# Performance work log

Measured on AMD Instinct MI355X. Metric: run time of the kernel, lower is better.

Reference implementation:

```python
import jax, jax.numpy as jnp
import numpy as np

H = 1024  # hidden_size
IN = 1    # input_size
OUT = 1   # out_size


def _lstm_cell(x, h, c, W_ih, W_hh, b_ih, b_hh):
    # PyTorch LSTMCell: gates ordered (i, f, g, o)
    gates = x @ W_ih.T + h @ W_hh.T + (b_ih + b_hh)
    i, f, g, o = jnp.split(gates, 4, axis=-1)
    c_new = jax.nn.sigmoid(f) * c + jax.nn.sigmoid(i) * jnp.tanh(g)
    h_new = jax.nn.sigmoid(o) * jnp.tanh(c_new)
    return h_new, c_new


def setup_inputs() -> dict:
    key = jax.random.key(0)
    ks = jax.random.split(key, 12)
    B, T = 128, 256
    s1 = 1.0 / np.sqrt(H)
    u = lambda k, shp: jax.random.uniform(k, shp, jnp.float32, -s1, s1)
    return {
        "x": jax.random.normal(ks[0], (B, T), jnp.float32),
        "W_ih1": u(ks[1], (4 * H, IN)),
        "W_hh1": u(ks[2], (4 * H, H)),
        "b_ih1": u(ks[3], (4 * H,)),
        "b_hh1": u(ks[4], (4 * H,)),
        "W_ih2": u(ks[5], (4 * H, H)),
        "W_hh2": u(ks[6], (4 * H, H)),
        "b_ih2": u(ks[7], (4 * H,)),
        "b_hh2": u(ks[8], (4 * H,)),
        "W_lin": u(ks[9], (OUT, H)),
        "b_lin": u(ks[10], (OUT,)),
        "future": 64,
    }


def reference(x, W_ih1, W_hh1, b_ih1, b_hh1, W_ih2, W_hh2, b_ih2, b_hh2,
              W_lin, b_lin, future):
    B = x.shape[0]
    z = jnp.zeros((B, H), x.dtype)
    carry0 = (z, z, z, z)
    xs = jnp.swapaxes(x, 0, 1)[:, :, None]  # [T, B, 1]

    def cell_stack(carry, inp):
        h1, c1, h2, c2 = carry
        h1, c1 = _lstm_cell(inp, h1, c1, W_ih1, W_hh1, b_ih1, b_hh1)
        h2, c2 = _lstm_cell(h1, h2, c2, W_ih2, W_hh2, b_ih2, b_hh2)
        out = h2 @ W_lin.T + b_lin  # [B, 1]
        return (h1, c1, h2, c2), out

    carry, outs = jax.lax.scan(cell_stack, carry0, xs)  # outs: [T, B, 1]

    if future > 0:
        def ar_step(carry, _):
            h1, c1, h2, c2, out = carry
            (h1, c1, h2, c2), new_out = cell_stack((h1, c1, h2, c2), out)
            return (h1, c1, h2, c2, new_out), new_out

        _, outs2 = jax.lax.scan(ar_step, (*carry, outs[-1]), None, length=future)
        outs = jnp.concatenate([outs, outs2], axis=0)

    return jnp.swapaxes(outs[..., 0], 0, 1)  # [B, T+future]
```

## Files before the change

kernel.cpp:

```cpp
#include <hip/hip_runtime.h>


typedef _Float16 f16;
typedef _Float16 f16x8 __attribute__((ext_vector_type(8)));
typedef _Float16 f16x4 __attribute__((ext_vector_type(4)));
typedef float    f32x4 __attribute__((ext_vector_type(4)));
typedef int      i32x4 __attribute__((ext_vector_type(4)));
typedef unsigned int   u32;
typedef unsigned short u16;

#define NB   256
#define WGS  512
#define HS   1024
#define BS   128
#define TS   256
#define TTS  320
#define KST  32
#define PSTR 131072

#define OFF_H1    0u
#define OFF_H2    524288u
#define OFF_CNT1  1572864u
#define OFF_CNT2  1835008u
#define OFF_FLAG  2097152u
#define OFF_XREG  2162688u
#define OFF_ACC   2163200u
#define WS_END    2196480u

#define NSLOT       64
#define SLOT_TGT    4
#define SLOT_STRIDE 1024

#define LDS_G1    131072
#define LDS_G2    139264
#define LDS_XF    147456
#define LDS_PRM   147968
#define LDS_MISC  148224
#define LDS_SH1   148352
#define LDS_SH2   149376
#define LDS_TOTAL 151552

__device__ __forceinline__ float sigm(float x){ return 1.0f/(1.0f + __expf(-x)); }

__device__ __forceinline__ void wt_store(u32* p, u32 v) {
  __hip_atomic_store(p, v, __ATOMIC_RELAXED, __HIP_MEMORY_SCOPE_AGENT);
}

__device__ __forceinline__ void st16_wt(f16* addr, f16x8 v) {
  i32x4 d = __builtin_bit_cast(i32x4, v);
  asm volatile("global_store_dwordx4 %0, %1, off sc0 sc1"
               :: "v"(addr), "v"(d) : "memory");
}

__device__ __forceinline__ void poll_slots(const int* cnt, int t) {
  const int* p = cnt + (threadIdx.x & 63) * SLOT_STRIDE + t;
  while (__hip_atomic_load(p, __ATOMIC_RELAXED, __HIP_MEMORY_SCOPE_AGENT) < SLOT_TGT)
    __builtin_amdgcn_s_sleep(1);
}

__global__ void init_ws_kernel(char* ws){
  const size_t n = (WS_END - OFF_CNT1) / 16u;
  float4* r = (float4*)(ws + OFF_CNT1);
  float4 z = make_float4(0.f, 0.f, 0.f, 0.f);
  size_t stride = (size_t)gridDim.x * blockDim.x;
  for (size_t i = blockIdx.x*(size_t)blockDim.x + threadIdx.x; i < n; i += stride) r[i] = z;
  __builtin_amdgcn_fence(__ATOMIC_RELEASE, "agent");
}

__global__ void __launch_bounds__(WGS, 2)
lstm_coop(const float* __restrict__ xg,
          const float* __restrict__ Wih1, const float* __restrict__ Whh1,
          const float* __restrict__ bih1, const float* __restrict__ bhh1,
          const float* __restrict__ Wih2, const float* __restrict__ Whh2,
          const float* __restrict__ bih2, const float* __restrict__ bhh2,
          const float* __restrict__ Wlin, const float* __restrict__ blin,
          float* __restrict__ outp, char* __restrict__ ws)
{
  extern __shared__ char smem[];
  f16*   Wlds = (f16*)smem;
  float* g1s  = (float*)(smem + LDS_G1);
  float* g2s  = (float*)(smem + LDS_G2);
  float* xfd  = (float*)(smem + LDS_XF);
  float* prm  = (float*)(smem + LDS_PRM);
  int*   miscl= (int*)(smem + LDS_MISC);
  f16*   sh1  = (f16*)(smem + LDS_SH1);
  f16*   sh2  = (f16*)(smem + LDS_SH2);

  f16* H1  = (f16*)(ws + OFF_H1);
  f16* H2  = (f16*)(ws + OFF_H2);
  int* cnt1 = (int*)(ws + OFF_CNT1);
  int* cnt2 = (int*)(ws + OFF_CNT2);
  int* flags= (int*)(ws + OFF_FLAG);
  float* accs = (float*)(ws + OFF_ACC);

  const int tid = threadIdx.x;
  const int blk = blockIdx.x;

  int xcd_raw;
  asm("s_getreg_b32 %0, hwreg(HW_REG_XCC_ID)" : "=s"(xcd_raw));
  if (tid == 0) {
    int x = xcd_raw & 7;
    int rank = __hip_atomic_fetch_add((int*)(ws + OFF_XREG) + x*16, 1,
                                      __ATOMIC_RELAXED, __HIP_MEMORY_SCOPE_AGENT);
    miscl[0] = x;
    miscl[1] = (rank == 0) ? 1 : 0;
  }

  for (int item = tid; item < 4*KST*64; item += WGS) {
    int tile = item >> 11;
    int rem  = item & 2047;
    int k0   = rem >> 6;
    int lane = rem & 63;
    int n    = lane & 15;
    int kbase = k0*32 + (lane>>4)*8;
    f16x8 pk;
    if (tile < 3) {
      const float* Wsrc = (tile==0) ? Whh1 : (tile==1) ? Wih2 : Whh2;
      const float* p = Wsrc + (size_t)((n>>2)*1024 + blk*4 + (n&3))*HS + kbase;
      #pragma unroll
      for (int j=0;j<8;j++) pk[j] = (f16)p[j];
    } else {
      #pragma unroll
      for (int j=0;j<8;j++) pk[j] = (n==0) ? (f16)Wlin[kbase+j] : (f16)0.0f;
    }
    *(f16x8*)(Wlds + (size_t)item*8) = pk;
  }
  if (tid < 16) {
    int row = (tid>>2)*1024 + blk*4 + (tid&3);
    prm[tid]      = Wih1[row];
    prm[16 + tid] = bih1[row] + bhh1[row];
    prm[32 + tid] = bih2[row] + bhh2[row];
  }
  if (tid == 16) prm[48] = blin[0];

  const int erow = tid >> 2;
  const int eu   = tid & 3;
  const float wlin_c = Wlin[blk*4 + eu];
  float c1 = 0.f, c2 = 0.f;
  __syncthreads();

  const int  myxcd  = miscl[0];
  const bool leader = miscl[1] != 0;
  int* flag = flags + myxcd * 2048;

  const int wv    = tid >> 6;
  const int lane  = tid & 63;
  const int n15   = lane & 15;
  const int mrow  = wv*16 + n15;
  const int kc    = (lane>>4)*8;
  const int rbase = wv*16 + (lane>>4)*4;
  const f16x8* WB = (const f16x8*)Wlds;
  const int abase = mrow*4 + (kc>>2)*512;

  for (int t = 0; t < TTS; ++t) {
    const int p1 = t & 1;
    const int p2 = (t + 1) & 1;

    if (t >= TS) {
      if (wv == 7) poll_slots(cnt2, t);
      __syncthreads();
      if (tid < BS) {
        float v = __hip_atomic_load(accs + (t-TS)*BS + tid,
                                    __ATOMIC_RELAXED, __HIP_MEMORY_SCOPE_AGENT) + prm[48];
        xfd[tid] = v;
        if (blk == ((t-1) & 255))
          wt_store((u32*)&outp[tid*TTS + (t-1)], __builtin_bit_cast(u32, v));
      }
      __syncthreads();
    }

    {
      float h1v;
      if (t == 0) {
        float xv = xg[erow*TS + 0];
        float gi = xv*prm[0*4+eu] + prm[16 + 0*4+eu];
        float gg = xv*prm[2*4+eu] + prm[16 + 2*4+eu];
        float go = xv*prm[3*4+eu] + prm[16 + 3*4+eu];
        c1 = sigm(gi)*tanhf(gg);
        h1v = sigm(go)*tanhf(c1);
      } else {
        float xv = (t < TS) ? xg[erow*TS + t] : xfd[erow];
        float gi = g1s[erow*16 + 0*4+eu] + xv*prm[0*4+eu];
        float gf = g1s[erow*16 + 1*4+eu] + xv*prm[1*4+eu];
        float gg = g1s[erow*16 + 2*4+eu] + xv*prm[2*4+eu];
        float go = g1s[erow*16 + 3*4+eu] + xv*prm[3*4+eu];
        c1 = sigm(gf)*c1 + sigm(gi)*tanhf(gg);
        h1v = sigm(go)*tanhf(c1);
      }
      sh1[tid] = (f16)h1v;
    }
    __syncthreads();

    if (wv == 0) {
      st16_wt(H1 + (size_t)p1*PSTR + blk*512 + lane*8,
              *(const f16x8*)(sh1 + lane*8));
      asm volatile("s_waitcnt vmcnt(0)" ::: "memory");
      if (lane == 0)
        __hip_atomic_fetch_add(cnt1 + (blk & (NSLOT-1))*SLOT_STRIDE + t, 1,
                               __ATOMIC_RELAXED, __HIP_MEMORY_SCOPE_AGENT);
    }

    if (wv == 7) {
      if (leader) {
        if (t >= 1) poll_slots(cnt2, t);
        poll_slots(cnt1, t);
        __builtin_amdgcn_fence(__ATOMIC_ACQUIRE, "agent");
        asm volatile("s_waitcnt vmcnt(0)" ::: "memory");
        if (lane == 0)
          __hip_atomic_store(flag, t + 1, __ATOMIC_RELAXED, __HIP_MEMORY_SCOPE_AGENT);
      } else {
        if (lane == 0) {
          while (__hip_atomic_load(flag, __ATOMIC_RELAXED, __HIP_MEMORY_SCOPE_AGENT) < t + 1)
            __builtin_amdgcn_s_sleep(1);
        }
      }
    }
    __syncthreads();

    const f16* A1 = H1 + (size_t)p1*PSTR + abase;
    const f16* A2 = H2 + (size_t)p2*PSTR + abase;
    f32x4 acc1  = {0.f,0.f,0.f,0.f};
    f32x4 acc2a = {0.f,0.f,0.f,0.f};
    f32x4 acc2b = {0.f,0.f,0.f,0.f};
    f32x4 accO  = {0.f,0.f,0.f,0.f};
    if (t == 0) {
      #pragma unroll 8
      for (int k0 = 0; k0 < KST; ++k0) {
        f16x4 a1l = *(const f16x4*)(A1 + k0*4096);
        f16x4 a1h = *(const f16x4*)(A1 + k0*4096 + 512);
        f16x8 a1  = __builtin_shufflevector(a1l, a1h, 0,1,2,3,4,5,6,7);
        f16x8 b0 = WB[(0*KST + k0)*64 + lane];
        f16x8 b1 = WB[(1*KST + k0)*64 + lane];
        acc1  = __builtin_amdgcn_mfma_f32_16x16x32_f16(a1, b0, acc1,  0,0,0);
        acc2a = __builtin_amdgcn_mfma_f32_16x16x32_f16(a1, b1, acc2a, 0,0,0);
      }
    } else {
      #pragma unroll 8
      for (int k0 = 0; k0 < KST; ++k0) {
        f16x4 a1l = *(const f16x4*)(A1 + k0*4096);
        f16x4 a1h = *(const f16x4*)(A1 + k0*4096 + 512);
        f16x4 a2l = *(const f16x4*)(A2 + k0*4096);
        f16x4 a2h = *(const f16x4*)(A2 + k0*4096 + 512);
        f16x8 a1  = __builtin_shufflevector(a1l, a1h, 0,1,2,3,4,5,6,7);
        f16x8 a2  = __builtin_shufflevector(a2l, a2h, 0,1,2,3,4,5,6,7);
        f16x8 b0 = WB[(0*KST + k0)*64 + lane];
        f16x8 b1 = WB[(1*KST + k0)*64 + lane];
        f16x8 b2 = WB[(2*KST + k0)*64 + lane];
        f16x8 b3 = WB[(3*KST + k0)*64 + lane];
        acc1  = __builtin_amdgcn_mfma_f32_16x16x32_f16(a1, b0, acc1,  0,0,0);
        acc2a = __builtin_amdgcn_mfma_f32_16x16x32_f16(a1, b1, acc2a, 0,0,0);
        acc2b = __builtin_amdgcn_mfma_f32_16x16x32_f16(a2, b2, acc2b, 0,0,0);
        accO  = __builtin_amdgcn_mfma_f32_16x16x32_f16(a2, b3, accO,  0,0,0);
      }
    }
    #pragma unroll
    for (int r = 0; r < 4; ++r) {
      int grow = rbase + r;
      g1s[grow*16 + n15] = acc1[r]  + prm[16 + n15];
      g2s[grow*16 + n15] = acc2a[r] + acc2b[r] + prm[32 + n15];
    }
    if (n15 == 0 && blk == ((t-1) & 255) && t >= 1 && t <= TS-1) {
      #pragma unroll
      for (int r = 0; r < 4; ++r)
        wt_store((u32*)&outp[(rbase+r)*TTS + (t-1)],
                 __builtin_bit_cast(u32, accO[r] + prm[48]));
    }
    __syncthreads();

    {
      float gi = g2s[erow*16 + 0*4+eu];
      float gf = g2s[erow*16 + 1*4+eu];
      float gg = g2s[erow*16 + 2*4+eu];
      float go = g2s[erow*16 + 3*4+eu];
      c2 = sigm(gf)*c2 + sigm(gi)*tanhf(gg);
      float h2v = sigm(go)*tanhf(c2);
      sh2[tid] = (f16)h2v;
      if (t >= TS-1) {
        float p = h2v * wlin_c;
        p += __shfl_xor(p, 1);
        p += __shfl_xor(p, 2);
        if (eu == 0)
          __hip_atomic_fetch_add(accs + (t-(TS-1))*BS + erow, p,
                                 __ATOMIC_RELAXED, __HIP_MEMORY_SCOPE_AGENT);
      }
    }
    if (t >= TS-1)
      asm volatile("s_waitcnt vmcnt(0)" ::: "memory");
    __syncthreads();

    if (wv == 1) {
      st16_wt(H2 + (size_t)p1*PSTR + blk*512 + lane*8,
              *(const f16x8*)(sh2 + lane*8));
      asm volatile("s_waitcnt vmcnt(0)" ::: "memory");
      if (lane == 0)
        __hip_atomic_fetch_add(cnt2 + (blk & (NSLOT-1))*SLOT_STRIDE + (t+1), 1,
                               __ATOMIC_RELAXED, __HIP_MEMORY_SCOPE_AGENT);
    }
  }

  if (blk == 63) {
    if (wv == 7) poll_slots(cnt2, TTS);
    __syncthreads();
    if (tid < BS) {
      float v = __hip_atomic_load(accs + (TTS-TS)*BS + tid,
                                  __ATOMIC_RELAXED, __HIP_MEMORY_SCOPE_AGENT) + prm[48];
      wt_store((u32*)&outp[tid*TTS + (TTS-1)], __builtin_bit_cast(u32, v));
    }
  }
}

extern "C" void kernel_launch(void* const* d_in, const int* in_sizes, int n_in,
                              void* d_out, int out_size, void* d_ws, size_t ws_size,
                              hipStream_t stream) {
  const float* xg   = (const float*)d_in[0];
  const float* Wih1 = (const float*)d_in[1];
  const float* Whh1 = (const float*)d_in[2];
  const float* bih1 = (const float*)d_in[3];
  const float* bhh1 = (const float*)d_in[4];
  const float* Wih2 = (const float*)d_in[5];
  const float* Whh2 = (const float*)d_in[6];
  const float* bih2 = (const float*)d_in[7];
  const float* bhh2 = (const float*)d_in[8];
  const float* Wlin = (const float*)d_in[9];
  const float* blin = (const float*)d_in[10];
  float* outp = (float*)d_out;
  char* ws = (char*)d_ws;

  init_ws_kernel<<<dim3(128), dim3(256), 0, stream>>>(ws);

  (void)hipFuncSetAttribute((const void*)lstm_coop,
                            hipFuncAttributeMaxDynamicSharedMemorySize, LDS_TOTAL);

  void* args[] = { (void*)&xg, (void*)&Wih1, (void*)&Whh1, (void*)&bih1, (void*)&bhh1,
                   (void*)&Wih2, (void*)&Whh2, (void*)&bih2, (void*)&bhh2,
                   (void*)&Wlin, (void*)&blin, (void*)&outp, (void*)&ws };
  hipError_t err = hipLaunchCooperativeKernel((const void*)lstm_coop,
                                              dim3(NB), dim3(WGS), args, LDS_TOTAL, stream);
  if (err != hipSuccess) {
    lstm_coop<<<dim3(NB), dim3(WGS), LDS_TOTAL, stream>>>(
        xg, Wih1, Whh1, bih1, bhh1, Wih2, Whh2, bih2, bhh2, Wlin, blin, outp, ws);
  }
}
```

Measured before the change: 4.690 ms.

## Overlap next-step layer-1 cell with layer-2 and use atomic linear head

Measured after the change: 7.005 ms. +49.4%, slower.

```diff
diff --git a/kernel.cpp b/kernel.cpp
--- a/kernel.cpp
+++ b/kernel.cpp
@@ -17,28 +17,29 @@
 #define TTS  320
 #define KST  32
 #define PSTR 131072
+#define NT   3
 
 #define OFF_H1    0u
 #define OFF_H2    524288u
-#define OFF_CNT1  1572864u
-#define OFF_CNT2  1835008u
-#define OFF_FLAG  2097152u
-#define OFF_XREG  2162688u
-#define OFF_ACC   2163200u
-#define WS_END    2196480u
+#define OFF_CNT1  1048576u
+#define OFF_CNT2  1310720u
+#define OFF_FLAG  1572864u
+#define OFF_XREG  1638400u
+#define OFF_ACC   1638912u
+#define WS_END    1802752u
 
 #define NSLOT       64
 #define SLOT_TGT    4
 #define SLOT_STRIDE 1024
 
-#define LDS_G1    131072
-#define LDS_G2    139264
-#define LDS_XF    147456
-#define LDS_PRM   147968
-#define LDS_MISC  148224
-#define LDS_SH1   148352
-#define LDS_SH2   149376
-#define LDS_TOTAL 151552
+#define LDS_G1    98304
+#define LDS_G2    106496
+#define LDS_XF    114688
+#define LDS_PRM   115200
+#define LDS_MISC  115456
+#define LDS_SH1   115584
+#define LDS_SH2   116608
+#define LDS_TOTAL 117760
 
 __device__ __forceinline__ float sigm(float x){ return 1.0f/(1.0f + __expf(-x)); }
 
@@ -106,23 +107,18 @@
     miscl[1] = (rank == 0) ? 1 : 0;
   }
 
-  for (int item = tid; item < 4*KST*64; item += WGS) {
+  for (int item = tid; item < NT*KST*64; item += WGS) {
     int tile = item >> 11;
     int rem  = item & 2047;
     int k0   = rem >> 6;
     int lane = rem & 63;
     int n    = lane & 15;
     int kbase = k0*32 + (lane>>4)*8;
+    const float* Wsrc = (tile==0) ? Whh1 : (tile==1) ? Wih2 : Whh2;
+    const float* p = Wsrc + (size_t)((n>>2)*1024 + blk*4 + (n&3))*HS + kbase;
     f16x8 pk;
-    if (tile < 3) {
-      const float* Wsrc = (tile==0) ? Whh1 : (tile==1) ? Wih2 : Whh2;
-      const float* p = Wsrc + (size_t)((n>>2)*1024 + blk*4 + (n&3))*HS + kbase;
-      #pragma unroll
-      for (int j=0;j<8;j++) pk[j] = (f16)p[j];
-    } else {
-      #pragma unroll
-      for (int j=0;j<8;j++) pk[j] = (n==0) ? (f16)Wlin[kbase+j] : (f16)0.0f;
-    }
+    #pragma unroll
+    for (int j=0;j<8;j++) pk[j] = (f16)p[j];
     *(f16x8*)(Wlds + (size_t)item*8) = pk;
   }
   if (tid < 16) {
@@ -152,6 +148,24 @@
   const f16x8* WB = (const f16x8*)Wlds;
   const int abase = mrow*4 + (kc>>2)*512;
 
+  {
+    float xv = xg[erow*TS + 0];
+    float gi = xv*prm[0*4+eu] + prm[16 + 0*4+eu];
+    float gg = xv*prm[2*4+eu] + prm[16 + 2*4+eu];
+    float go = xv*prm[3*4+eu] + prm[16 + 3*4+eu];
+    c1 = sigm(gi)*tanhf(gg);
+    float h1v = sigm(go)*tanhf(c1);
+    sh1[tid] = (f16)h1v;
+  }
+  __syncthreads();
+  if (wv == 0) {
+    st16_wt(H1 + (size_t)0*PSTR + blk*512 + lane*8, *(const f16x8*)(sh1 + lane*8));
+    asm volatile("s_waitcnt vmcnt(0)" ::: "memory");
+    if (lane == 0)
+      __hip_atomic_fetch_add(cnt1 + (blk & (NSLOT-1))*SLOT_STRIDE + 0, 1,
+                             __ATOMIC_RELAXED, __HIP_MEMORY_SCOPE_AGENT);
+  }
+
   for (int t = 0; t < TTS; ++t) {
     const int p1 = t & 1;
     const int p2 = (t + 1) & 1;
@@ -159,45 +173,28 @@
     if (t >= TS) {
       if (wv == 7) poll_slots(cnt2, t);
       __syncthreads();
-      if (tid < BS) {
-        float v = __hip_atomic_load(accs + (t-TS)*BS + tid,
-                                    __ATOMIC_RELAXED, __HIP_MEMORY_SCOPE_AGENT) + prm[48];
-        xfd[tid] = v;
-        if (blk == ((t-1) & 255))
-          wt_store((u32*)&outp[tid*TTS + (t-1)], __builtin_bit_cast(u32, v));
-      }
+      if (tid < BS)
+        xfd[tid] = __hip_atomic_load(accs + (size_t)(t-1)*BS + tid,
+                                     __ATOMIC_RELAXED, __HIP_MEMORY_SCOPE_AGENT) + prm[48];
       __syncthreads();
-    }
-
-    {
-      float h1v;
-      if (t == 0) {
-        float xv = xg[erow*TS + 0];
-        float gi = xv*prm[0*4+eu] + prm[16 + 0*4+eu];
-        float gg = xv*prm[2*4+eu] + prm[16 + 2*4+eu];
-        float go = xv*prm[3*4+eu] + prm[16 + 3*4+eu];
-        c1 = sigm(gi)*tanhf(gg);
-        h1v = sigm(go)*tanhf(c1);
-      } else {
-        float xv = (t < TS) ? xg[erow*TS + t] : xfd[erow];
+      {
+        float xv = xfd[erow];
         float gi = g1s[erow*16 + 0*4+eu] + xv*prm[0*4+eu];
         float gf = g1s[erow*16 + 1*4+eu] + xv*prm[1*4+eu];
         float gg = g1s[erow*16 + 2*4+eu] + xv*prm[2*4+eu];
         float go = g1s[erow*16 + 3*4+eu] + xv*prm[3*4+eu];
         c1 = sigm(gf)*c1 + sigm(gi)*tanhf(gg);
-        h1v = sigm(go)*tanhf(c1);
-      }
-      sh1[tid] = (f16)h1v;
-    }
-    __syncthreads();
-
-    if (wv == 0) {
-      st16_wt(H1 + (size_t)p1*PSTR + blk*512 + lane*8,
-              *(const f16x8*)(sh1 + lane*8));
-      asm volatile("s_waitcnt vmcnt(0)" ::: "memory");
-      if (lane == 0)
-        __hip_atomic_fetch_add(cnt1 + (blk & (NSLOT-1))*SLOT_STRIDE + t, 1,
-                               __ATOMIC_RELAXED, __HIP_MEMORY_SCOPE_AGENT);
+        float h1v = sigm(go)*tanhf(c1);
+        sh1[tid] = (f16)h1v;
+      }
+      __syncthreads();
+      if (wv == 0) {
+        st16_wt(H1 + (size_t)p1*PSTR + blk*512 + lane*8, *(const f16x8*)(sh1 + lane*8));
+        asm volatile("s_waitcnt vmcnt(0)" ::: "memory");
+        if (lane == 0)
+          __hip_atomic_fetch_add(cnt1 + (blk & (NSLOT-1))*SLOT_STRIDE + t, 1,
+                                 __ATOMIC_RELAXED, __HIP_MEMORY_SCOPE_AGENT);
+      }
     }
 
     if (wv == 7) {
@@ -217,40 +214,45 @@
     }
     __syncthreads();
 
+    if (t >= 1 && blk == ((t-1) & 255) && tid < BS) {
+      float v = __hip_atomic_load(accs + (size_t)(t-1)*BS + tid,
+                                  __ATOMIC_RELAXED, __HIP_MEMORY_SCOPE_AGENT) + prm[48];
+      wt_store((u32*)&outp[tid*TTS + (t-1)], __builtin_bit_cast(u32, v));
+    }
+
+    float xv_next = 0.0f;
+    if (t + 1 <= TS-1) xv_next = xg[erow*TS + (t+1)];
+
+    f16x8 h2r[KST];
+    const f16* A2 = H2 + (size_t)p2*PSTR + abase;
+    if (t >= 1) {
+      #pragma unroll
+      for (int k0 = 0; k0 < KST; ++k0) {
+        f16x4 lo = *(const f16x4*)(A2 + k0*4096);
+        f16x4 hi = *(const f16x4*)(A2 + k0*4096 + 512);
+        h2r[k0] = __builtin_shufflevector(lo, hi, 0,1,2,3,4,5,6,7);
+      }
+    }
+
     const f16* A1 = H1 + (size_t)p1*PSTR + abase;
-    const f16* A2 = H2 + (size_t)p2*PSTR + abase;
     f32x4 acc1  = {0.f,0.f,0.f,0.f};
     f32x4 acc2a = {0.f,0.f,0.f,0.f};
     f32x4 acc2b = {0.f,0.f,0.f,0.f};
-    f32x4 accO  = {0.f,0.f,0.f,0.f};
-    if (t == 0) {
-      #pragma unroll 8
+    #pragma unroll 8
+    for (int k0 = 0; k0 < KST; ++k0) {
+      f16x4 a1l = *(const f16x4*)(A1 + k0*4096);
+      f16x4 a1h = *(const f16x4*)(A1 + k0*4096 + 512);
+      f16x8 a1  = __builtin_shufflevector(a1l, a1h, 0,1,2,3,4,5,6,7);
+      f16x8 b0 = WB[(0*KST + k0)*64 + lane];
+      f16x8 b1 = WB[(1*KST + k0)*64 + lane];
+      acc1  = __builtin_amdgcn_mfma_f32_16x16x32_f16(a1, b0, acc1,  0,0,0);
+      acc2a = __builtin_amdgcn_mfma_f32_16x16x32_f16(a1, b1, acc2a, 0,0,0);
+    }
+    if (t >= 1) {
+      #pragma unroll
       for (int k0 = 0; k0 < KST; ++k0) {
-        f16x4 a1l = *(const f16x4*)(A1 + k0*4096);
-        f16x4 a1h = *(const f16x4*)(A1 + k0*4096 + 512);
-        f16x8 a1  = __builtin_shufflevector(a1l, a1h, 0,1,2,3,4,5,6,7);
-        f16x8 b0 = WB[(0*KST + k0)*64 + lane];
-        f16x8 b1 = WB[(1*KST + k0)*64 + lane];
-        acc1  = __builtin_amdgcn_mfma_f32_16x16x32_f16(a1, b0, acc1,  0,0,0);
-        acc2a = __builtin_amdgcn_mfma_f32_16x16x32_f16(a1, b1, acc2a, 0,0,0);
-      }
-    } else {
-      #pragma unroll 8
-      for (int k0 = 0; k0 < KST; ++k0) {
-        f16x4 a1l = *(const f16x4*)(A1 + k0*4096);
-        f16x4 a1h = *(const f16x4*)(A1 + k0*4096 + 512);
-        f16x4 a2l = *(const f16x4*)(A2 + k0*4096);
-        f16x4 a2h = *(const f16x4*)(A2 + k0*4096 + 512);
-        f16x8 a1  = __builtin_shufflevector(a1l, a1h, 0,1,2,3,4,5,6,7);
-        f16x8 a2  = __builtin_shufflevector(a2l, a2h, 0,1,2,3,4,5,6,7);
-        f16x8 b0 = WB[(0*KST + k0)*64 + lane];
-        f16x8 b1 = WB[(1*KST + k0)*64 + lane];
         f16x8 b2 = WB[(2*KST + k0)*64 + lane];
-        f16x8 b3 = WB[(3*KST + k0)*64 + lane];
-        acc1  = __builtin_amdgcn_mfma_f32_16x16x32_f16(a1, b0, acc1,  0,0,0);
-        acc2a = __builtin_amdgcn_mfma_f32_16x16x32_f16(a1, b1, acc2a, 0,0,0);
-        acc2b = __builtin_amdgcn_mfma_f32_16x16x32_f16(a2, b2, acc2b, 0,0,0);
-        accO  = __builtin_amdgcn_mfma_f32_16x16x32_f16(a2, b3, accO,  0,0,0);
+        acc2b = __builtin_amdgcn_mfma_f32_16x16x32_f16(h2r[k0], b2, acc2b, 0,0,0);
       }
     }
     #pragma unroll
@@ -258,12 +260,6 @@
       int grow = rbase + r;
       g1s[grow*16 + n15] = acc1[r]  + prm[16 + n15];
       g2s[grow*16 + n15] = acc2a[r] + acc2b[r] + prm[32 + n15];
-    }
-    if (n15 == 0 && blk == ((t-1) & 255) && t >= 1 && t <= TS-1) {
-      #pragma unroll
-      for (int r = 0; r < 4; ++r)
-        wt_store((u32*)&outp[(rbase+r)*TTS + (t-1)],
-                 __builtin_bit_cast(u32, accO[r] + prm[48]));
     }
     __syncthreads();
 
@@ -275,22 +271,37 @@
       c2 = sigm(gf)*c2 + sigm(gi)*tanhf(gg);
       float h2v = sigm(go)*tanhf(c2);
       sh2[tid] = (f16)h2v;
-      if (t >= TS-1) {
-        float p = h2v * wlin_c;
-        p += __shfl_xor(p, 1);
-        p += __shfl_xor(p, 2);
-        if (eu == 0)
-          __hip_atomic_fetch_add(accs + (t-(TS-1))*BS + erow, p,
-                                 __ATOMIC_RELAXED, __HIP_MEMORY_SCOPE_AGENT);
-      }
-    }
-    if (t >= TS-1)
+      float p = h2v * wlin_c;
+      p += __shfl_xor(p, 1);
+      p += __shfl_xor(p, 2);
+      if (eu == 0)
+        __hip_atomic_fetch_add(accs + (size_t)t*BS + erow, p,
+                               __ATOMIC_RELAXED, __HIP_MEMORY_SCOPE_AGENT);
+    }
+
+    if (t + 1 <= TS-1) {
+      float xv = xv_next;
+      float gi = g1s[erow*16 + 0*4+eu] + xv*prm[0*4+eu];
+      float gf = g1s[erow*16 + 1*4+eu] + xv*prm[1*4+eu];
+      float gg = g1s[erow*16 + 2*4+eu] + xv*prm[2*4+eu];
+      float go = g1s[erow*16 + 3*4+eu] + xv*prm[3*4+eu];
+      c1 = sigm(gf)*c1 + sigm(gi)*tanhf(gg);
+      float h1v = sigm(go)*tanhf(c1);
+      sh1[tid] = (f16)h1v;
+    }
+
+    asm volatile("s_waitcnt vmcnt(0)" ::: "memory");
+    __syncthreads();
+
+    if (wv == 0 && t + 1 <= TS-1) {
+      st16_wt(H1 + (size_t)p2*PSTR + blk*512 + lane*8, *(const f16x8*)(sh1 + lane*8));
       asm volatile("s_waitcnt vmcnt(0)" ::: "memory");
-    __syncthreads();
-
+      if (lane == 0)
+        __hip_atomic_fetch_add(cnt1 + (blk & (NSLOT-1))*SLOT_STRIDE + (t+1), 1,
+                               __ATOMIC_RELAXED, __HIP_MEMORY_SCOPE_AGENT);
+    }
     if (wv == 1) {
-      st16_wt(H2 + (size_t)p1*PSTR + blk*512 + lane*8,
-              *(const f16x8*)(sh2 + lane*8));
+      st16_wt(H2 + (size_t)p1*PSTR + blk*512 + lane*8, *(const f16x8*)(sh2 + lane*8));
       asm volatile("s_waitcnt vmcnt(0)" ::: "memory");
       if (lane == 0)
         __hip_atomic_fetch_add(cnt2 + (blk & (NSLOT-1))*SLOT_STRIDE + (t+1), 1,
@@ -302,7 +313,7 @@
     if (wv == 7) poll_slots(cnt2, TTS);
     __syncthreads();
     if (tid < BS) {
-      float v = __hip_atomic_load(accs + (TTS-TS)*BS + tid,
+      float v = __hip_atomic_load(accs + (size_t)(TTS-1)*BS + tid,
                                   __ATOMIC_RELAXED, __HIP_MEMORY_SCOPE_AGENT) + prm[48];
       wt_store((u32*)&outp[tid*TTS + (TTS-1)], __builtin_bit_cast(u32, v));
     }
```

## Compute output projection via per-XCD atomic partial sums instead of MFMA tile

Applied to the files above, without the earlier changes.

Result: no change. 4.634 ms (-1.2%).

```diff
diff --git a/kernel.cpp b/kernel.cpp
--- a/kernel.cpp
+++ b/kernel.cpp
@@ -7,7 +7,6 @@
 typedef float    f32x4 __attribute__((ext_vector_type(4)));
 typedef int      i32x4 __attribute__((ext_vector_type(4)));
 typedef unsigned int   u32;
-typedef unsigned short u16;
 
 #define NB   256
 #define WGS  512
@@ -17,28 +16,29 @@
 #define TTS  320
 #define KST  32
 #define PSTR 131072
+#define NT   3
 
 #define OFF_H1    0u
 #define OFF_H2    524288u
-#define OFF_CNT1  1572864u
-#define OFF_CNT2  1835008u
-#define OFF_FLAG  2097152u
-#define OFF_XREG  2162688u
-#define OFF_ACC   2163200u
-#define WS_END    2196480u
+#define OFF_CNT1  1048576u
+#define OFF_CNT2  1179648u
+#define OFF_FLAG  1310720u
+#define OFF_XREG  1376256u
+#define OFF_ACC8  1376768u
+#define WS_END    2687488u
 
 #define NSLOT       64
 #define SLOT_TGT    4
-#define SLOT_STRIDE 1024
-
-#define LDS_G1    131072
-#define LDS_G2    139264
-#define LDS_XF    147456
-#define LDS_PRM   147968
-#define LDS_MISC  148224
-#define LDS_SH1   148352
-#define LDS_SH2   149376
-#define LDS_TOTAL 151552
+#define SLOT_STRIDE 512
+
+#define LDS_G1    98304
+#define LDS_G2    106496
+#define LDS_XF    114688
+#define LDS_PRM   115200
+#define LDS_MISC  115456
+#define LDS_SH1   115584
+#define LDS_SH2   116608
+#define LDS_TOTAL 117760
 
 __device__ __forceinline__ float sigm(float x){ return 1.0f/(1.0f + __expf(-x)); }
 
@@ -91,7 +91,7 @@
   int* cnt1 = (int*)(ws + OFF_CNT1);
   int* cnt2 = (int*)(ws + OFF_CNT2);
   int* flags= (int*)(ws + OFF_FLAG);
-  float* accs = (float*)(ws + OFF_ACC);
+  float* accs8 = (float*)(ws + OFF_ACC8);
 
   const int tid = threadIdx.x;
   const int blk = blockIdx.x;
@@ -106,23 +106,18 @@
     miscl[1] = (rank == 0) ? 1 : 0;
   }
 
-  for (int item = tid; item < 4*KST*64; item += WGS) {
+  for (int item = tid; item < NT*KST*64; item += WGS) {
     int tile = item >> 11;
     int rem  = item & 2047;
     int k0   = rem >> 6;
     int lane = rem & 63;
     int n    = lane & 15;
     int kbase = k0*32 + (lane>>4)*8;
+    const float* Wsrc = (tile==0) ? Whh1 : (tile==1) ? Wih2 : Whh2;
+    const float* p = Wsrc + (size_t)((n>>2)*1024 + blk*4 + (n&3))*HS + kbase;
     f16x8 pk;
-    if (tile < 3) {
-      const float* Wsrc = (tile==0) ? Whh1 : (tile==1) ? Wih2 : Whh2;
-      const float* p = Wsrc + (size_t)((n>>2)*1024 + blk*4 + (n&3))*HS + kbase;
-      #pragma unroll
-      for (int j=0;j<8;j++) pk[j] = (f16)p[j];
-    } else {
-      #pragma unroll
-      for (int j=0;j<8;j++) pk[j] = (n==0) ? (f16)Wlin[kbase+j] : (f16)0.0f;
-    }
+    #pragma unroll
+    for (int j=0;j<8;j++) pk[j] = (f16)p[j];
     *(f16x8*)(Wlds + (size_t)item*8) = pk;
   }
   if (tid < 16) {
@@ -142,6 +137,7 @@
   const int  myxcd  = miscl[0];
   const bool leader = miscl[1] != 0;
   int* flag = flags + myxcd * 2048;
+  float* myacc = accs8 + (size_t)myxcd * TTS * BS;
 
   const int wv    = tid >> 6;
   const int lane  = tid & 63;
@@ -160,11 +156,12 @@
       if (wv == 7) poll_slots(cnt2, t);
       __syncthreads();
       if (tid < BS) {
-        float v = __hip_atomic_load(accs + (t-TS)*BS + tid,
-                                    __ATOMIC_RELAXED, __HIP_MEMORY_SCOPE_AGENT) + prm[48];
-        xfd[tid] = v;
-        if (blk == ((t-1) & 255))
-          wt_store((u32*)&outp[tid*TTS + (t-1)], __builtin_bit_cast(u32, v));
+        float s = 0.f;
+        #pragma unroll
+        for (int x = 0; x < 8; ++x)
+          s += __hip_atomic_load(accs8 + ((size_t)x*TTS + (t-1))*BS + tid,
+                                 __ATOMIC_RELAXED, __HIP_MEMORY_SCOPE_AGENT);
+        xfd[tid] = s + prm[48];
       }
       __syncthreads();
     }
@@ -192,8 +189,7 @@
     __syncthreads();
 
     if (wv == 0) {
-      st16_wt(H1 + (size_t)p1*PSTR + blk*512 + lane*8,
-              *(const f16x8*)(sh1 + lane*8));
+      st16_wt(H1 + (size_t)p1*PSTR + blk*512 + lane*8, *(const f16x8*)(sh1 + lane*8));
       asm volatile("s_waitcnt vmcnt(0)" ::: "memory");
       if (lane == 0)
         __hip_atomic_fetch_add(cnt1 + (blk & (NSLOT-1))*SLOT_STRIDE + t, 1,
@@ -217,12 +213,26 @@
     }
     __syncthreads();
 
+    if (t >= 1 && blk == ((t-1) & 255) && tid < BS) {
+      float v;
+      if (t >= TS) {
+        v = xfd[tid];
+      } else {
+        float s = 0.f;
+        #pragma unroll
+        for (int x = 0; x < 8; ++x)
+          s += __hip_atomic_load(accs8 + ((size_t)x*TTS + (t-1))*BS + tid,
+                                 __ATOMIC_RELAXED, __HIP_MEMORY_SCOPE_AGENT);
+        v = s + prm[48];
+      }
+      wt_store((u32*)&outp[tid*TTS + (t-1)], __builtin_bit_cast(u32, v));
+    }
+
     const f16* A1 = H1 + (size_t)p1*PSTR + abase;
     const f16* A2 = H2 + (size_t)p2*PSTR + abase;
     f32x4 acc1  = {0.f,0.f,0.f,0.f};
     f32x4 acc2a = {0.f,0.f,0.f,0.f};
     f32x4 acc2b = {0.f,0.f,0.f,0.f};
-    f32x4 accO  = {0.f,0.f,0.f,0.f};
     if (t == 0) {
       #pragma unroll 8
       for (int k0 = 0; k0 < KST; ++k0) {
@@ -246,11 +256,9 @@
         f16x8 b0 = WB[(0*KST + k0)*64 + lane];
         f16x8 b1 = WB[(1*KST + k0)*64 + lane];
         f16x8 b2 = WB[(2*KST + k0)*64 + lane];
-        f16x8 b3 = WB[(3*KST + k0)*64 + lane];
         acc1  = __builtin_amdgcn_mfma_f32_16x16x32_f16(a1, b0, acc1,  0,0,0);
         acc2a = __builtin_amdgcn_mfma_f32_16x16x32_f16(a1, b1, acc2a, 0,0,0);
         acc2b = __builtin_amdgcn_mfma_f32_16x16x32_f16(a2, b2, acc2b, 0,0,0);
-        accO  = __builtin_amdgcn_mfma_f32_16x16x32_f16(a2, b3, accO,  0,0,0);
       }
     }
     #pragma unroll
@@ -258,12 +266,6 @@
       int grow = rbase + r;
       g1s[grow*16 + n15] = acc1[r]  + prm[16 + n15];
       g2s[grow*16 + n15] = acc2a[r] + acc2b[r] + prm[32 + n15];
-    }
-    if (n15 == 0 && blk == ((t-1) & 255) && t >= 1 && t <= TS-1) {
-      #pragma unroll
-      for (int r = 0; r < 4; ++r)
-        wt_store((u32*)&outp[(rbase+r)*TTS + (t-1)],
-                 __builtin_bit_cast(u32, accO[r] + prm[48]));
     }
     __syncthreads();
 
@@ -275,22 +277,19 @@
       c2 = sigm(gf)*c2 + sigm(gi)*tanhf(gg);
       float h2v = sigm(go)*tanhf(c2);
       sh2[tid] = (f16)h2v;
-      if (t >= TS-1) {
-        float p = h2v * wlin_c;
-        p += __shfl_xor(p, 1);
-        p += __shfl_xor(p, 2);
-        if (eu == 0)
-          __hip_atomic_fetch_add(accs + (t-(TS-1))*BS + erow, p,
-                                 __ATOMIC_RELAXED, __HIP_MEMORY_SCOPE_AGENT);
-      }
-    }
-    if (t >= TS-1)
-      asm volatile("s_waitcnt vmcnt(0)" ::: "memory");
+      float p = h2v * wlin_c;
+      p += __shfl_xor(p, 1);
+      p += __shfl_xor(p, 2);
+      if (eu == 0)
+        __hip_atomic_fetch_add(myacc + (size_t)t*BS + erow, p,
+                               __ATOMIC_RELAXED, __HIP_MEMORY_SCOPE_AGENT);
+    }
+
+    asm volatile("s_waitcnt vmcnt(0)" ::: "memory");
     __syncthreads();
 
     if (wv == 1) {
-      st16_wt(H2 + (size_t)p1*PSTR + blk*512 + lane*8,
-              *(const f16x8*)(sh2 + lane*8));
+      st16_wt(H2 + (size_t)p1*PSTR + blk*512 + lane*8, *(const f16x8*)(sh2 + lane*8));
       asm volatile("s_waitcnt vmcnt(0)" ::: "memory");
       if (lane == 0)
         __hip_atomic_fetch_add(cnt2 + (blk & (NSLOT-1))*SLOT_STRIDE + (t+1), 1,
@@ -302,9 +301,13 @@
     if (wv == 7) poll_slots(cnt2, TTS);
     __syncthreads();
     if (tid < BS) {
-      float v = __hip_atomic_load(accs + (TTS-TS)*BS + tid,
-                                  __ATOMIC_RELAXED, __HIP_MEMORY_SCOPE_AGENT) + prm[48];
-      wt_store((u32*)&outp[tid*TTS + (TTS-1)], __builtin_bit_cast(u32, v));
+      float s = 0.f;
+      #pragma unroll
+      for (int x = 0; x < 8; ++x)
+        s += __hip_atomic_load(accs8 + ((size_t)x*TTS + (TTS-1))*BS + tid,
+                               __ATOMIC_RELAXED, __HIP_MEMORY_SCOPE_AGENT);
+      wt_store((u32*)&outp[tid*TTS + (TTS-1)],
+               __builtin_bit_cast(u32, s + prm[48]));
     }
   }
 }
```
